# Optimization experiments

Hardware: AMD Instinct MI355X
Metric: run time of the kernel (lower is better)

## Reference

```python
import jax, jax.numpy as jnp
import numpy as np

H = 128; D = 16; L = 4
NP_ = 50000; NL_ = 10000; EPP = 500000; ELP = 100000; EPL = 100000


def _rbf(d):
    # GaussianSmearing(start=0, stop=8, num_gaussians=16)
    off = jnp.linspace(0.0, 8.0, D)
    coeff = -0.5 / ((8.0 / (D - 1)) ** 2)
    x = d[:, None] - off[None, :]
    return jnp.exp(coeff * x * x)


def _layer_norm(x, w, b, eps=1e-5):
    mu = jnp.mean(x, axis=-1, keepdims=True)
    var = jnp.var(x, axis=-1, keepdims=True)
    return (x - mu) * jax.lax.rsqrt(var + eps) * w + b


def _block(x_src, x_dst, src, dst, ea, Wf_, bf_, Ws_, bs_, bnw, bnb, lnw, lnb):
    # CGConv message: z = [x_i(dst), x_j(src), edge_attr]
    z = jnp.concatenate([x_dst[dst], x_src[src], ea], axis=-1)  # [E, 2H+D]
    m = jax.nn.sigmoid(z @ Wf_ + bf_) * jax.nn.softplus(z @ Ws_ + bs_)
    agg = jax.ops.segment_sum(m, dst, num_segments=x_dst.shape[0])
    # BatchNorm1d in eval mode with running_mean=0, running_var=1
    agg = agg * (bnw / jnp.sqrt(1.0 + 1e-5)) + bnb
    out = agg + x_dst            # CGConv internal residual
    out = _layer_norm(out, lnw, lnb)
    out = jax.nn.relu(out)
    return out + x_dst           # ResidualCGConvBlock residual (dropout=identity in eval)


def setup_inputs() -> dict:
    key = jax.random.key(0)
    ks = jax.random.split(key, 16)
    s = lambda n: 1.0 / np.sqrt(n)
    inp = {
        'x_protein': jax.random.normal(ks[0], (NP_, 6), jnp.float32),
        'x_ligand': jax.random.normal(ks[1], (NL_, 6), jnp.float32),
        'ei_pp': jnp.stack([jax.random.randint(ks[2], (EPP,), 0, NP_),
                            jax.random.randint(ks[3], (EPP,), 0, NP_)]).astype(jnp.int32),
        'ea_pp': jax.random.uniform(ks[4], (EPP,), jnp.float32, 0.0, 8.0),
        'ei_lp': jnp.stack([jax.random.randint(ks[5], (ELP,), 0, NL_),
                            jax.random.randint(ks[6], (ELP,), 0, NP_)]).astype(jnp.int32),
        'ea_lp': jax.random.uniform(ks[7], (ELP,), jnp.float32, 0.0, 8.0),
        'ei_pl': jnp.stack([jax.random.randint(ks[8], (EPL,), 0, NP_),
                            jax.random.randint(ks[9], (EPL,), 0, NL_)]).astype(jnp.int32),
        'ea_pl': jax.random.uniform(ks[10], (EPL,), jnp.float32, 0.0, 8.0),
        'Wp': jax.random.normal(ks[11], (6, H), jnp.float32) * s(6),
        'bp': jnp.zeros((H,), jnp.float32),
        'Wl': jax.random.normal(ks[12], (6, H), jnp.float32) * s(6),
        'bl': jnp.zeros((H,), jnp.float32),
        'Wf': jax.random.normal(ks[13], (L, 3, 2 * H + D, H), jnp.float32) * s(2 * H + D),
        'bf': jnp.zeros((L, 3, H), jnp.float32),
        'Ws': jax.random.normal(ks[14], (L, 3, 2 * H + D, H), jnp.float32) * s(2 * H + D),
        'bs': jnp.zeros((L, 3, H), jnp.float32),
        'bn_w': jnp.ones((L, 3, H), jnp.float32),
        'bn_b': jnp.zeros((L, 3, H), jnp.float32),
        'ln_w': jnp.ones((L, 3, H), jnp.float32),
        'ln_b': jnp.zeros((L, 3, H), jnp.float32),
        'lno_w': jnp.ones((H,), jnp.float32),
        'lno_b': jnp.zeros((H,), jnp.float32),
        'fc_w': jax.random.normal(ks[15], (H, 21), jnp.float32) * s(H),
        'fc_b': jnp.zeros((21,), jnp.float32),
    }
    return inp


def reference(x_protein, x_ligand, ei_pp, ea_pp, ei_lp, ea_lp, ei_pl, ea_pl,
              Wp, bp, Wl, bl, Wf, bf, Ws, bs, bn_w, bn_b, ln_w, ln_b,
              lno_w, lno_b, fc_w, fc_b):
    xp = x_protein @ Wp + bp
    xl = x_ligand @ Wl + bl
    rpp = _rbf(ea_pp); rlp = _rbf(ea_lp); rpl = _rbf(ea_pl)
    for l in range(L):
        # HeteroConv aggr='sum': protein receives from pp and lp; ligand from pl
        p_pp = _block(xp, xp, ei_pp[0], ei_pp[1], rpp, Wf[l, 0], bf[l, 0], Ws[l, 0], bs[l, 0],
                      bn_w[l, 0], bn_b[l, 0], ln_w[l, 0], ln_b[l, 0])
        p_lp = _block(xl, xp, ei_lp[0], ei_lp[1], rlp, Wf[l, 1], bf[l, 1], Ws[l, 1], bs[l, 1],
                      bn_w[l, 1], bn_b[l, 1], ln_w[l, 1], ln_b[l, 1])
        l_pl = _block(xp, xl, ei_pl[0], ei_pl[1], rpl, Wf[l, 2], bf[l, 2], Ws[l, 2], bs[l, 2],
                      bn_w[l, 2], bn_b[l, 2], ln_w[l, 2], ln_b[l, 2])
        xp, xl = p_pp + p_lp, l_pl
    out = _layer_norm(xp, lno_w, lno_b)
    return out @ fc_w + fc_b
```

## Files before the change

### kernel.cpp

```cpp
#include <hip/hip_runtime.h>
#include <hip/hip_bf16.h>
#include <math.h>

#define H 128
#define LOG2E 1.44269504f

typedef __bf16 bf16x8 __attribute__((ext_vector_type(8)));
typedef float f32x4 __attribute__((ext_vector_type(4)));
typedef float f32x2 __attribute__((ext_vector_type(2)));
typedef __hip_bfloat16 bf16;
typedef unsigned int uint32;

static __device__ __forceinline__ float bf2f(bf16 v){ return __bfloat162float(v); }
static __device__ __forceinline__ bf16 f2bf(float v){ return __float2bfloat16(v); }
static __device__ __forceinline__ float u2f_lo(uint32 v){ return __uint_as_float(v << 16); }
static __device__ __forceinline__ float u2f_hi(uint32 v){ return __uint_as_float(v & 0xffff0000u); }

union bfpack { struct { bf16 lo, hi; } h; uint32 u; };
static __device__ __forceinline__ uint32 pack_bf2(float a, float b){
  bfpack p; p.h.lo = f2bf(a); p.h.hi = f2bf(b); return p.u;
}

static __device__ __forceinline__ int unperm64(int r){
  int base = r & ~63; int g = r & 63; int t = g >> 4; int j = g & 15;
  return base + 4*j + t;
}

#define NBIN 256
#define PREP_WP_N (4*1024*128)
#define PREP_WL_N (4*512*128)
#define RBF_N     (12*(NBIN+1)*128)

__global__ void prep_all(const float* __restrict__ Wf, const float* __restrict__ Ws,
                         const float* __restrict__ bfv, const float* __restrict__ bsv,
                         bf16* __restrict__ Wt_p, float* __restrict__ Bias_p,
                         bf16* __restrict__ Wt_l, float* __restrict__ Bias_l,
                         bf16* __restrict__ T2,
                         const float* __restrict__ Xp, const float* __restrict__ Wp,
                         const float* __restrict__ bp, float* __restrict__ Xpo,
                         bf16* __restrict__ Xpb, int NP,
                         const float* __restrict__ Xl, const float* __restrict__ Wl,
                         const float* __restrict__ bl, float* __restrict__ Xlo,
                         bf16* __restrict__ Xlb, int NL){
  int t = blockIdx.x*blockDim.x + threadIdx.x;
  if (t < PREP_WP_N){
    int k = t & 127; int idx = t >> 7;
    int rs = idx & 1023; int l = idx >> 10;
    int r = unperm64(rs);
    int rel, c, row0; const float* W; float bias = 0.f;
    if (r < 256)      { rel=0; c=r>>1;        row0=128; W = (r&1)?Ws:Wf; }
    else if (r < 512) { rel=2; c=(r-256)>>1;  row0=128; W = (r&1)?Ws:Wf; }
    else if (r < 640) { rel=0; c=r-512; row0=0; W=Wf; bias = bfv[(l*3+rel)*H+c]; }
    else if (r < 768) { rel=0; c=r-640; row0=0; W=Ws; bias = bsv[(l*3+rel)*H+c]; }
    else if (r < 896) { rel=1; c=r-768; row0=0; W=Wf; bias = bfv[(l*3+rel)*H+c]; }
    else              { rel=1; c=r-896; row0=0; W=Ws; bias = bsv[(l*3+rel)*H+c]; }
    Wt_p[t] = f2bf(LOG2E * W[((size_t)(l*3+rel)*272 + row0 + k)*H + c]);
    if (k == 0) Bias_p[l*1024 + r] = LOG2E * bias;
    return;
  }
  t -= PREP_WP_N;
  if (t < PREP_WL_N){
    int k = t & 127; int idx = t >> 7;
    int rs = idx & 511; int l = idx >> 9;
    int r = unperm64(rs);
    int rel, c, row0; const float* W; float bias = 0.f;
    if (r < 256)      { rel=1; c=r>>1;   row0=128; W = (r&1)?Ws:Wf; }
    else if (r < 384) { rel=2; c=r-256; row0=0; W=Wf; bias = bfv[(l*3+rel)*H+c]; }
    else              { rel=2; c=r-384; row0=0; W=Ws; bias = bsv[(l*3+rel)*H+c]; }
    Wt_l[t] = f2bf(LOG2E * W[((size_t)(l*3+rel)*272 + row0 + k)*H + c]);
    if (k == 0) Bias_l[l*512 + r] = LOG2E * bias;
    return;
  }
  t -= PREP_WL_N;
  if (t < RBF_N){
    int c = t & 127;
    int b = (t >> 7) % (NBIN+1);
    int pr = t / ((NBIN+1)*128);
    float d0 = (float)b * (8.0f/(float)NBIN);
    const float* wf = Wf + ((size_t)pr*272 + 256)*H + c;
    const float* ws = Ws + ((size_t)pr*272 + 256)*H + c;
    float f0=0.f, s0=0.f;
    #pragma unroll
    for (int k=0;k<16;k++){
      float o = 0.533333333f*(float)k;
      float tt = d0 - o;
      float r0 = __expf(-1.7578125f*tt*tt);
      f0 += r0*wf[(size_t)k*H]; s0 += r0*ws[(size_t)k*H];
    }
    bf16* o = T2 + ((size_t)(pr*(NBIN+1) + b))*256 + 2*c;
    o[0]=f2bf(LOG2E * f0); o[1]=f2bf(LOG2E * s0);
    return;
  }
  t -= RBF_N;
  {
    int idx = t;
    const float* Xin; const float* W; const float* b; float* Xout; bf16* Xbf;
    if (idx < NP*H){ Xin=Xp; W=Wp; b=bp; Xout=Xpo; Xbf=Xpb; }
    else { idx -= NP*H; if (idx >= NL*H) return; Xin=Xl; W=Wl; b=bl; Xout=Xlo; Xbf=Xlb; }
    int n = idx >> 7, c = idx & 127;
    float acc = b[c];
    #pragma unroll
    for (int k=0;k<6;k++) acc += Xin[n*6+k] * W[k*H+c];
    Xout[idx] = acc;
    Xbf[idx] = f2bf(acc);
  }
}

__global__ void hist3_k(const int* __restrict__ dpp, int Epp,
                        const int* __restrict__ dlp, int Elp,
                        const int* __restrict__ dpl, int Epl,
                        int* __restrict__ cpp, int* __restrict__ clp, int* __restrict__ cpl){
  int e = blockIdx.x*blockDim.x + threadIdx.x;
  if (e < Epp) atomicAdd(&cpp[dpp[e]], 1);
  else if (e < Epp+Elp) atomicAdd(&clp[dlp[e-Epp]], 1);
  else if (e < Epp+Elp+Epl) atomicAdd(&cpl[dpl[e-Epp-Elp]], 1);
}

#define SCH 1024

__global__ void __launch_bounds__(256) chunksum_k(
    const int* __restrict__ counts, int NP, int NL, int Cpp, int Cpl,
    int* __restrict__ chsum){
  __shared__ int wred[4];
  int b = blockIdx.x;
  const int* cnt; int n; int ch;
  if (b < Cpp){ cnt = counts; n = NP; ch = b; }
  else if (b < 2*Cpp){ cnt = counts + NP; n = NP; ch = b - Cpp; }
  else { cnt = counts + 2*NP; n = NL; ch = b - 2*Cpp; }
  int base = ch * SCH;
  int tid = threadIdx.x;
  int s = 0;
  #pragma unroll
  for (int j=0;j<SCH/256;j++){
    int i = base + tid + j*256;
    if (i < n) s += cnt[i];
  }
  #pragma unroll
  for (int o=32;o>=1;o>>=1) s += __shfl_xor(s,o,64);
  if ((tid & 63) == 0) wred[tid>>6] = s;
  __syncthreads();
  if (tid == 0) chsum[b] = wred[0]+wred[1]+wred[2]+wred[3];
}

__global__ void __launch_bounds__(192) scanmid_k(
    int* __restrict__ chsum, int Cpp, int Cpl, int NP, int NL,
    int* __restrict__ rp_pp, int* __restrict__ rp_lp, int* __restrict__ rp_pl){
  int wid = threadIdx.x >> 6, lane = threadIdx.x & 63;
  int C, off; int* rp_end; int n;
  if (wid == 0){ C = Cpp; off = 0;      rp_end = rp_pp; n = NP; }
  else if (wid == 1){ C = Cpp; off = Cpp; rp_end = rp_lp; n = NP; }
  else { C = Cpl; off = 2*Cpp; rp_end = rp_pl; n = NL; }
  int v = (lane < C) ? chsum[off + lane] : 0;
  int x = v;
  #pragma unroll
  for (int o=1;o<64;o<<=1){
    int y = __shfl_up(x, o, 64);
    if (lane >= o) x += y;
// ... 79 lines not shown
    if (d > 63) d = 63;
    atomicAdd(&lh[64 + 63 - d], 1);
  }
  __syncthreads();
  if (t < 128 && lh[t]) atomicAdd(&hist[t], lh[t]);
}

__global__ void __launch_bounds__(128) degbin_scan(
    const int* __restrict__ hist, int* __restrict__ cursor){
  int t = threadIdx.x, lane = t & 63;
  int v = hist[t];
  int x = v;
  #pragma unroll
  for (int o=1;o<64;o<<=1){
    int y = __shfl_up(x, o, 64);
    if (lane >= o) x += y;
  }
  cursor[t] = x - v;
}

__global__ void __launch_bounds__(256) degbin_scatter(
    const int* __restrict__ rp_pp, const int* __restrict__ rp_lp,
    const int* __restrict__ rp_pl, int NP, int NL,
    int* __restrict__ cursor, int* __restrict__ perm){
  __shared__ int lh[128], lbase[128], lrank[128];
  int t = threadIdx.x;
  if (t < 128){ lh[t] = 0; lrank[t] = 0; }
  __syncthreads();
  int i = blockIdx.x*256 + t;
  int bin = -1, n = 0;
  if (i < NP){
    n = i;
    int d = (rp_pp[i+1]-rp_pp[i]) + (rp_lp[i+1]-rp_lp[i]);
    if (d > 63) d = 63;
    bin = 63 - d;
  } else if (i < NP+NL){
    n = i - NP;
    int d = rp_pl[n+1]-rp_pl[n];
    if (d > 63) d = 63;
    bin = 64 + 63 - d;
  }
  if (bin >= 0) atomicAdd(&lh[bin], 1);
  __syncthreads();
  if (t < 128 && lh[t]) lbase[t] = atomicAdd(&cursor[t], lh[t]);
  __syncthreads();
  if (bin >= 0){
    int r = atomicAdd(&lrank[bin], 1);
    perm[(bin < 64 ? 0 : NP) + lbase[bin] + r] = n;
  }
}

#define GR 8
__global__ void __launch_bounds__(256) gemm_tables(
    const bf16* __restrict__ Xp, const bf16* __restrict__ Wtp,
    const float* __restrict__ Biasp, bf16* __restrict__ Outp,
    int strips_p, int tasks_p,
    const bf16* __restrict__ Xl, const bf16* __restrict__ Wtl,
    const float* __restrict__ Biasl, bf16* __restrict__ Outl,
    int strips_l, int tasks_total){
  int wt = blockIdx.x*4 + (threadIdx.x >> 6);
  if (wt >= tasks_total) return;
  const bf16 *X, *Wt; const float* Bias; bf16* Out; int N, strips, g, chunk;
  if (wt < tasks_p){
    X=Xp; Wt=Wtp; Bias=Biasp; Out=Outp; N=1024; strips=strips_p;
    g = wt & 15; chunk = wt >> 4;
  } else {
    int w = wt - tasks_p;
    X=Xl; Wt=Wtl; Bias=Biasl; Out=Outl; N=512; strips=strips_l;
    g = w & 7; chunk = w >> 3;
  }
  int n0 = g << 6;
  int lane = threadIdx.x & 63;
  int lr = lane & 15, lq = lane >> 4;
  const bf16x8* B0 = (const bf16x8*)(const void*)(Wt + (size_t)(n0      + lr)*H);
  const bf16x8* B1 = (const bf16x8*)(const void*)(Wt + (size_t)(n0 + 16 + lr)*H);
  const bf16x8* B2 = (const bf16x8*)(const void*)(Wt + (size_t)(n0 + 32 + lr)*H);
  const bf16x8* B3 = (const bf16x8*)(const void*)(Wt + (size_t)(n0 + 48 + lr)*H);
  bf16x8 b0_0=B0[lq], b0_1=B0[4+lq], b0_2=B0[8+lq], b0_3=B0[12+lq];
  bf16x8 b1_0=B1[lq], b1_1=B1[4+lq], b1_2=B1[8+lq], b1_3=B1[12+lq];
  bf16x8 b2_0=B2[lq], b2_1=B2[4+lq], b2_2=B2[8+lq], b2_3=B2[12+lq];
  bf16x8 b3_0=B3[lq], b3_1=B3[4+lq], b3_2=B3[8+lq], b3_3=B3[12+lq];
  float4 bias = ((const float4*)(const void*)(Bias + n0))[lr];
  #pragma unroll 2
  for (int r=0;r<GR;r++){
    int strip = chunk*GR + r;
    if (strip >= strips) break;
    int m0 = strip << 4;
    const bf16x8* A = (const bf16x8*)(const void*)(X + (size_t)(m0+lr)*H);
    bf16x8 a0 = A[lq], a1 = A[4+lq], a2 = A[8+lq], a3 = A[12+lq];
    f32x4 acc0 = {0.f,0.f,0.f,0.f}, acc1 = acc0, acc2 = acc0, acc3 = acc0;
    acc0 = __builtin_amdgcn_mfma_f32_16x16x32_bf16(a0, b0_0, acc0, 0, 0, 0);
    acc1 = __builtin_amdgcn_mfma_f32_16x16x32_bf16(a0, b1_0, acc1, 0, 0, 0);
    acc2 = __builtin_amdgcn_mfma_f32_16x16x32_bf16(a0, b2_0, acc2, 0, 0, 0);
    acc3 = __builtin_amdgcn_mfma_f32_16x16x32_bf16(a0, b3_0, acc3, 0, 0, 0);
    acc0 = __builtin_amdgcn_mfma_f32_16x16x32_bf16(a1, b0_1, acc0, 0, 0, 0);
    acc1 = __builtin_amdgcn_mfma_f32_16x16x32_bf16(a1, b1_1, acc1, 0, 0, 0);
    acc2 = __builtin_amdgcn_mfma_f32_16x16x32_bf16(a1, b2_1, acc2, 0, 0, 0);
    acc3 = __builtin_amdgcn_mfma_f32_16x16x32_bf16(a1, b3_1, acc3, 0, 0, 0);
    acc0 = __builtin_amdgcn_mfma_f32_16x16x32_bf16(a2, b0_2, acc0, 0, 0, 0);
    acc1 = __builtin_amdgcn_mfma_f32_16x16x32_bf16(a2, b1_2, acc1, 0, 0, 0);
    acc2 = __builtin_amdgcn_mfma_f32_16x16x32_bf16(a2, b2_2, acc2, 0, 0, 0);
    acc3 = __builtin_amdgcn_mfma_f32_16x16x32_bf16(a2, b3_2, acc3, 0, 0, 0);
    acc0 = __builtin_amdgcn_mfma_f32_16x16x32_bf16(a3, b0_3, acc0, 0, 0, 0);
    acc1 = __builtin_amdgcn_mfma_f32_16x16x32_bf16(a3, b1_3, acc1, 0, 0, 0);
    acc2 = __builtin_amdgcn_mfma_f32_16x16x32_bf16(a3, b2_3, acc2, 0, 0, 0);
    acc3 = __builtin_amdgcn_mfma_f32_16x16x32_bf16(a3, b3_3, acc3, 0, 0, 0);
    #pragma unroll
    for (int rr=0;rr<4;rr++){
      int row = m0 + lq*4 + rr;
      uint2 pk;
      pk.x = pack_bf2(acc0[rr] + bias.x, acc1[rr] + bias.y);
      pk.y = pack_bf2(acc2[rr] + bias.z, acc3[rr] + bias.w);
      *(uint2*)(void*)(Out + (size_t)row*N + n0 + 4*lr) = pk;
    }
  }
}

static __device__ __forceinline__ float act_msg(float F, float S){
  float sig = __builtin_amdgcn_rcpf(1.f + __builtin_amdgcn_exp2f(-F));
  float e   = __builtin_amdgcn_exp2f(fminf(S, 86.f));
  float sp  = 0.69314718f * __builtin_amdgcn_logf(1.f + e);
  return sig * sp;
}

#define BN_RSQ 0.9999950000374997f

static __device__ __forceinline__ void edge_nb(uint2 g, uint2 t,
                                               f32x2 fd2, f32x2 sd2, f32x2& acc){
  f32x2 f2, s2;
  f2.x = u2f_lo(g.x) + u2f_lo(t.x);
  f2.y = u2f_lo(g.y) + u2f_lo(t.y);
  s2.x = u2f_hi(g.x) + u2f_hi(t.x);
  s2.y = u2f_hi(g.y) + u2f_hi(t.y);
  f2 += fd2; s2 += sd2;
  acc.x += act_msg(f2.x, s2.x);
  acc.y += act_msg(f2.y, s2.y);
}

static __device__ __forceinline__ void ln_stats_w(float v0, float v1, float& mu, float& var){
  float s = v0 + v1, q = v0*v0 + v1*v1;
  #pragma unroll
  for (int o=32;o>=1;o>>=1){ s += __shfl_xor(s,o,64); q += __shfl_xor(q,o,64); }
  mu = s * (1.f/128.f);
  var = q * (1.f/128.f) - mu*mu;
}

static __device__ __forceinline__ void aggregate(
    const int2* __restrict__ ev_arr, int e0, int e1,
    const uint2* __restrict__ G, int gstride, int goff,
    const uint2* __restrict__ Tb, int lane,
    f32x2 fd2, f32x2 sd2, f32x2& acc)
{
  for (int base = e0; base < e1; base += 64){
    int idx = base + lane;
    int2 ev = ev_arr[(idx < e1) ? idx : (e1-1)];
    float dd = __int_as_float(ev.y);
    int bnv = (int)__fmaf_rn(dd, (float)NBIN/8.0f, 0.5f);
    bnv = (bnv > NBIN) ? NBIN : bnv;
    int cnt = e1 - base; cnt = (cnt > 64) ? 64 : cnt;
    uint2 gA, tA, gB, tB, gC, tC;
    #define LDJ(gX, tX, j) { \
      int s_ = __builtin_amdgcn_readlane(ev.x, (j)); \
      int b_ = __builtin_amdgcn_readlane(bnv, (j)); \
      gX = G[(size_t)s_*gstride + goff + lane]; \
      tX = Tb[(size_t)b_*64 + lane]; }
    LDJ(gA, tA, 0);
    if (cnt > 1) LDJ(gB, tB, 1);
    if (cnt > 2) LDJ(gC, tC, 2);
    int j = 0;
    for (; j+5 < cnt; j += 3){
      edge_nb(gA, tA, fd2, sd2, acc); LDJ(gA, tA, j+3);
      edge_nb(gB, tB, fd2, sd2, acc); LDJ(gB, tB, j+4);
      edge_nb(gC, tC, fd2, sd2, acc); LDJ(gC, tC, j+5);
    }
    int rem = cnt - j;
    edge_nb(gA, tA, fd2, sd2, acc);
    if (rem > 3) LDJ(gA, tA, j+3);
    if (rem > 1) edge_nb(gB, tB, fd2, sd2, acc);
    if (rem > 4) LDJ(gB, tB, j+4);
    if (rem > 2) edge_nb(gC, tC, fd2, sd2, acc);
    if (rem > 3) edge_nb(gA, tA, fd2, sd2, acc);
    if (rem > 4) edge_nb(gB, tB, fd2, sd2, acc);
    #undef LDJ
  }
}

__global__ void __launch_bounds__(256) node_update(
    const bf16* __restrict__ PT, const bf16* __restrict__ LT,
    const float* __restrict__ xp, const float* __restrict__ xl,
    const int* __restrict__ pp_rp, const int2* __restrict__ pp_e2,
    const int* __restrict__ lp_rp, const int2* __restrict__ lp_e2,
    const int* __restrict__ pl_rp, const int2* __restrict__ pl_e2,
    const bf16* __restrict__ T2,
    const float* __restrict__ bn_w, const float* __restrict__ bn_b,
    const float* __restrict__ ln_w, const float* __restrict__ ln_b,
    const int* __restrict__ perm,
    float* __restrict__ xp_out, bf16* __restrict__ xp_bf,
    float* __restrict__ xl_out, bf16* __restrict__ xl_bf,
    int layer, int NP, int NL, int PB)
{
  int wave = threadIdx.x >> 6;
  int lane = threadIdx.x & 63;
  const uint2* PTg = (const uint2*)(const void*)PT;
  if ((int)blockIdx.x < PB){
    int idx = blockIdx.x*4 + wave;
    if (idx >= NP) return;
    int node = perm[idx];
    float2 x = ((const float2*)(const void*)(xp + (size_t)node*H))[lane];
    const uint32* PTu = (const uint32*)(const void*)PT;
    const uint2*  LTg = (const uint2*)(const void*)LT;
    float o1_0, o1_1, o2_0, o2_1;
    {
      int pr = layer*3 + 0;
      uint32 fdp = PTu[(size_t)node*512 + 256 + lane];
      uint32 sdp = PTu[(size_t)node*512 + 320 + lane];
      const uint2* Tb = (const uint2*)(const void*)(T2 + (size_t)pr*(NBIN+1)*256);
      f32x2 fd2 = {u2f_lo(fdp), u2f_hi(fdp)};
      f32x2 sd2 = {u2f_lo(sdp), u2f_hi(sdp)};
      f32x2 acc = {0.f, 0.f};
      aggregate(pp_e2, pp_rp[node], pp_rp[node+1], PTg, 256, 0, Tb, lane, fd2, sd2, acc);
      float2 bw = ((const float2*)(const void*)(bn_w + pr*H))[lane];
      float2 bb = ((const float2*)(const void*)(bn_b + pr*H))[lane];
      float2 lw = ((const float2*)(const void*)(ln_w + pr*H))[lane];
      float2 lb = ((const float2*)(const void*)(ln_b + pr*H))[lane];
      float v0 = acc.x * (bw.x * BN_RSQ) + bb.x + x.x;
      float v1 = acc.y * (bw.y * BN_RSQ) + bb.y + x.y;
      float mu, var; ln_stats_w(v0, v1, mu, var);
      float rs = rsqrtf(var + 1e-5f);
      o1_0 = fmaxf((v0-mu)*rs*lw.x + lb.x, 0.f) + x.x;
      o1_1 = fmaxf((v1-mu)*rs*lw.y + lb.y, 0.f) + x.y;
    }
    {
      int pr = layer*3 + 1;
      uint32 fdp = PTu[(size_t)node*512 + 384 + lane];
      uint32 sdp = PTu[(size_t)node*512 + 448 + lane];
      const uint2* Tb = (const uint2*)(const void*)(T2 + (size_t)pr*(NBIN+1)*256);
      f32x2 fd2 = {u2f_lo(fdp), u2f_hi(fdp)};
      f32x2 sd2 = {u2f_lo(sdp), u2f_hi(sdp)};
      f32x2 acc = {0.f, 0.f};
      aggregate(lp_e2, lp_rp[node], lp_rp[node+1], LTg, 128, 0, Tb, lane, fd2, sd2, acc);
      float2 bw = ((const float2*)(const void*)(bn_w + pr*H))[lane];
      float2 bb = ((const float2*)(const void*)(bn_b + pr*H))[lane];
      float2 lw = ((const float2*)(const void*)(ln_w + pr*H))[lane];
      float2 lb = ((const float2*)(const void*)(ln_b + pr*H))[lane];
      float v0 = acc.x * (bw.x * BN_RSQ) + bb.x + x.x;
      float v1 = acc.y * (bw.y * BN_RSQ) + bb.y + x.y;
      float mu, var; ln_stats_w(v0, v1, mu, var);
      float rs = rsqrtf(var + 1e-5f);
      o2_0 = fmaxf((v0-mu)*rs*lw.x + lb.x, 0.f) + x.x;
      o2_1 = fmaxf((v1-mu)*rs*lw.y + lb.y, 0.f) + x.y;
    }
    float out0 = o1_0 + o2_0, out1 = o1_1 + o2_1;
    ((float2*)(void*)(xp_out + (size_t)node*H))[lane] = make_float2(out0, out1);
    ((uint32*)(void*)(xp_bf + (size_t)node*H))[lane] = pack_bf2(out0, out1);
  } else {
    int idx = (blockIdx.x - PB)*4 + wave;
    if (idx >= NL) return;
    int node = perm[NP + idx];
    float2 x = ((const float2*)(const void*)(xl + (size_t)node*H))[lane];
    const uint32* LTu = (const uint32*)(const void*)LT;
    int pr = layer*3 + 2;
    uint32 fdp = LTu[(size_t)node*256 + 128 + lane];
    uint32 sdp = LTu[(size_t)node*256 + 192 + lane];
    const uint2* Tb = (const uint2*)(const void*)(T2 + (size_t)pr*(NBIN+1)*256);
    f32x2 fd2 = {u2f_lo(fdp), u2f_hi(fdp)};
    f32x2 sd2 = {u2f_lo(sdp), u2f_hi(sdp)};
    f32x2 acc = {0.f, 0.f};
    aggregate(pl_e2, pl_rp[node], pl_rp[node+1], PTg, 256, 64, Tb, lane, fd2, sd2, acc);
    float2 bw = ((const float2*)(const void*)(bn_w + pr*H))[lane];
    float2 bb = ((const float2*)(const void*)(bn_b + pr*H))[lane];
    float2 lw = ((const float2*)(const void*)(ln_w + pr*H))[lane];
    float2 lb = ((const float2*)(const void*)(ln_b + pr*H))[lane];
    float v0 = acc.x * (bw.x * BN_RSQ) + bb.x + x.x;
    float v1 = acc.y * (bw.y * BN_RSQ) + bb.y + x.y;
    float mu, var; ln_stats_w(v0, v1, mu, var);
    float rs = rsqrtf(var + 1e-5f);
    float out0 = fmaxf((v0-mu)*rs*lw.x + lb.x, 0.f) + x.x;
    float out1 = fmaxf((v1-mu)*rs*lw.y + lb.y, 0.f) + x.y;
    ((float2*)(void*)(xl_out + (size_t)node*H))[lane] = make_float2(out0, out1);
    ((uint32*)(void*)(xl_bf + (size_t)node*H))[lane] = pack_bf2(out0, out1);
  }
}

__global__ void __launch_bounds__(128) final_k(const float* __restrict__ xp,
    const float* __restrict__ lnw, const float* __restrict__ lnb,
    const float* __restrict__ fcw, const float* __restrict__ fcb,
    float* __restrict__ out, int N){
  __shared__ float sm[4];
  __shared__ float lnv[128];
  int node = blockIdx.x, c = threadIdx.x;
  float v = xp[(size_t)node*H + c];
  float s = v, q = v*v;
  #pragma unroll
  for (int o=32;o>=1;o>>=1){ s += __shfl_xor(s,o,64); q += __shfl_xor(q,o,64); }
  __syncthreads();
  if ((c & 63) == 0){ sm[(c>>6)*2] = s; sm[(c>>6)*2+1] = q; }
  __syncthreads();
  float S = sm[0] + sm[2], Q = sm[1] + sm[3];
  float mu = S * (1.f/128.f);
  float var = Q * (1.f/128.f) - mu*mu;
  float ln = (v-mu)*rsqrtf(var+1e-5f)*lnw[c] + lnb[c];
  lnv[c] = ln;
  __syncthreads();
  if (c < 21){
    float a = fcb[c];
    #pragma unroll 4
    for (int i=0;i<128;i++) a += lnv[i]*fcw[i*21+c];
    out[(size_t)node*21 + c] = a;
  }
}

extern "C" void kernel_launch(void* const* d_in, const int* in_sizes, int n_in,
                              void* d_out, int out_size, void* d_ws, size_t ws_size,
                              hipStream_t stream){
  const float* x_protein = (const float*)d_in[0];
  const float* x_ligand  = (const float*)d_in[1];
  const int*   ei_pp = (const int*)d_in[2];
  const float* ea_pp = (const float*)d_in[3];
  const int*   ei_lp = (const int*)d_in[4];
  const float* ea_lp = (const float*)d_in[5];
  const int*   ei_pl = (const int*)d_in[6];
  const float* ea_pl = (const float*)d_in[7];
  const float* Wp  = (const float*)d_in[8];
  const float* bp  = (const float*)d_in[9];
  const float* Wl  = (const float*)d_in[10];
  const float* bl  = (const float*)d_in[11];
  const float* Wf  = (const float*)d_in[12];
  const float* bfv = (const float*)d_in[13];
  const float* Wsv = (const float*)d_in[14];
  const float* bsv = (const float*)d_in[15];
  const float* bn_w = (const float*)d_in[16];
  const float* bn_b = (const float*)d_in[17];
  const float* ln_w = (const float*)d_in[18];
  const float* ln_b = (const float*)d_in[19];
  const float* lno_w = (const float*)d_in[20];
  const float* lno_b = (const float*)d_in[21];
  const float* fc_w = (const float*)d_in[22];
  const float* fc_b = (const float*)d_in[23];

  int NP  = in_sizes[0]/6, NL = in_sizes[1]/6;
  int EPP = in_sizes[3], ELP = in_sizes[5], EPL = in_sizes[7];

  char* ws = (char*)d_ws;
  size_t off = 0;
  auto alloc = [&](size_t bytes)->void*{
    void* p = ws + off; off = (off + bytes + 255) & ~(size_t)255; return p;
  };

  float* xpA = (float*)alloc((size_t)NP*H*4);
  float* xpB = (float*)alloc((size_t)NP*H*4);
  float* xlA = (float*)alloc((size_t)NL*H*4);
  float* xlB = (float*)alloc((size_t)NL*H*4);
  bf16* xp_bf = (bf16*)alloc((size_t)NP*H*2);
  bf16* xl_bf = (bf16*)alloc((size_t)NL*H*2);
  bf16* PT    = (bf16*)alloc((size_t)NP*1024*2);
  bf16* LT    = (bf16*)alloc((size_t)NL*512*2);
  bf16* Wt_p  = (bf16*)alloc((size_t)4*1024*H*2);
  bf16* Wt_l  = (bf16*)alloc((size_t)4*512*H*2);
  float* Bias_p = (float*)alloc((size_t)4*1024*4);
  float* Bias_l = (float*)alloc((size_t)4*512*4);
  bf16* T2    = (bf16*)alloc((size_t)12*(NBIN+1)*256*2);
  int* counts = (int*)alloc((size_t)(2*NP+NL)*4);
  int* rp_pp  = (int*)alloc((size_t)(NP+1)*4);
  int* cur_pp = (int*)alloc((size_t)NP*4);
  int* rp_lp  = (int*)alloc((size_t)(NP+1)*4);
  int* cur_lp = (int*)alloc((size_t)NP*4);
  int* rp_pl  = (int*)alloc((size_t)(NL+1)*4);
  int* cur_pl = (int*)alloc((size_t)NL*4);
  int2* e2_pp = (int2*)alloc((size_t)EPP*8);
  int2* e2_lp = (int2*)alloc((size_t)ELP*8);
  int2* e2_pl = (int2*)alloc((size_t)EPL*8);
  int Cpp = (NP + SCH - 1) / SCH;
  int Cpl = (NL + SCH - 1) / SCH;
  int* chsum = (int*)alloc((size_t)(2*Cpp + Cpl)*4);
  int* dhist  = (int*)alloc(128*4);
  int* dcur   = (int*)alloc(128*4);
  int* perm   = (int*)alloc((size_t)(NP+NL)*4);
  (void)ws_size; (void)n_in; (void)out_size;

  size_t prep_total = (size_t)PREP_WP_N + PREP_WL_N + RBF_N + (size_t)(NP+NL)*H;
  prep_all<<<(prep_total+255)/256, 256, 0, stream>>>(Wf, Wsv, bfv, bsv,
      Wt_p, Bias_p, Wt_l, Bias_l, T2,
      x_protein, Wp, bp, xpA, xp_bf, NP,
      x_ligand,  Wl, bl, xlA, xl_bf, NL);
  hipMemsetAsync(counts, 0, (size_t)(2*NP+NL)*4, stream);
  hipMemsetAsync(dhist, 0, 128*4, stream);
  int* cnt_pp = counts; int* cnt_lp = counts + NP; int* cnt_pl = counts + 2*NP;
  int Etot = EPP + ELP + EPL;
  hist3_k<<<(Etot+255)/256, 256, 0, stream>>>(ei_pp+EPP, EPP, ei_lp+ELP, ELP, ei_pl+EPL, EPL,
                                              cnt_pp, cnt_lp, cnt_pl);
  chunksum_k<<<2*Cpp + Cpl, 256, 0, stream>>>(counts, NP, NL, Cpp, Cpl, chsum);
  scanmid_k<<<1, 192, 0, stream>>>(chsum, Cpp, Cpl, NP, NL, rp_pp, rp_lp, rp_pl);
  scanfin_k<<<2*Cpp + Cpl, 1024, 0, stream>>>(counts, NP, NL, Cpp, Cpl, chsum,
                                              rp_pp, cur_pp, rp_lp, cur_lp, rp_pl, cur_pl);
  fill3_k<<<(Etot+255)/256, 256, 0, stream>>>(ei_pp, ea_pp, EPP, ei_lp, ea_lp, ELP,
                                              ei_pl, ea_pl, EPL,
                                              cur_pp, e2_pp, cur_lp, e2_lp, cur_pl, e2_pl);
  int nbks = (NP + NL + 255) / 256;
  degbin_hist<<<nbks, 256, 0, stream>>>(rp_pp, rp_lp, rp_pl, NP, NL, dhist);
  degbin_scan<<<1, 128, 0, stream>>>(dhist, dcur);
  degbin_scatter<<<nbks, 256, 0, stream>>>(rp_pp, rp_lp, rp_pl, NP, NL, dcur, perm);

  float* xp_cur = xpA; float* xp_nxt = xpB;
  float* xl_cur = xlA; float* xl_nxt = xlB;
  int strips_p = NP >> 4, strips_l = NL >> 4;
  int tasks_p = 16 * ((strips_p + GR - 1) / GR);
  int tasks_l = 8  * ((strips_l + GR - 1) / GR);
  int tasks_total = tasks_p + tasks_l;
  int PB = (NP + 3) / 4, LB = (NL + 3) / 4;
  for (int l=0; l<4; l++){
    gemm_tables<<<(tasks_total+3)/4, 256, 0, stream>>>(
        xp_bf, Wt_p + (size_t)l*1024*H, Bias_p + l*1024, PT, strips_p, tasks_p,
        xl_bf, Wt_l + (size_t)l*512*H,  Bias_l + l*512,  LT, strips_l, tasks_total);
    node_update<<<PB + LB, 256, 0, stream>>>(PT, LT, xp_cur, xl_cur,
        rp_pp, e2_pp, rp_lp, e2_lp, rp_pl, e2_pl, T2,
        bn_w, bn_b, ln_w, ln_b, perm, xp_nxt, xp_bf, xl_nxt, xl_bf, l, NP, NL, PB);
    float* t;
    t = xp_cur; xp_cur = xp_nxt; xp_nxt = t;
    t = xl_cur; xl_cur = xl_nxt; xl_nxt = t;
  }

  final_k<<<NP, 128, 0, stream>>>(xp_cur, lno_w, lno_b, fc_w, fc_b, (float*)d_out, NP);
}
```

Baseline: 822.5 us.

## Switch node tables and features from bf16/fp32 to fp16 with packed half adds

Converts the per-layer gather tables, weights, RBF tables and node features from bf16 (plus an fp32 copy) to fp16. The GEMM now uses the f16 MFMA, and the per-edge message sum is done with packed half2 adds instead of unpacking to fp32. The separate fp32 feature buffers are dropped and the residual is read from fp16, which cuts memory traffic. The table column interleave is also reordered so that f and s halves pack into adjacent uint32 words. The cost is fp16 range and precision risk in the residual stream and in the pre-activation sums.

```diff
diff --git a/kernel.cpp b/kernel.cpp
--- a/kernel.cpp
+++ b/kernel.cpp
@@ -5,20 +5,17 @@
 #define H 128
 #define LOG2E 1.44269504f
 
-typedef __bf16 bf16x8 __attribute__((ext_vector_type(8)));
+typedef _Float16 f16;
+typedef _Float16 f16x2 __attribute__((ext_vector_type(2)));
+typedef _Float16 f16x8 __attribute__((ext_vector_type(8)));
 typedef float f32x4 __attribute__((ext_vector_type(4)));
 typedef float f32x2 __attribute__((ext_vector_type(2)));
-typedef __hip_bfloat16 bf16;
 typedef unsigned int uint32;
 
-static __device__ __forceinline__ float bf2f(bf16 v){ return __bfloat162float(v); }
-static __device__ __forceinline__ bf16 f2bf(float v){ return __float2bfloat16(v); }
-static __device__ __forceinline__ float u2f_lo(uint32 v){ return __uint_as_float(v << 16); }
-static __device__ __forceinline__ float u2f_hi(uint32 v){ return __uint_as_float(v & 0xffff0000u); }
-
-union bfpack { struct { bf16 lo, hi; } h; uint32 u; };
-static __device__ __forceinline__ uint32 pack_bf2(float a, float b){
-  bfpack p; p.h.lo = f2bf(a); p.h.hi = f2bf(b); return p.u;
+union u2h { uint32 u; f16x2 h; };
+static __device__ __forceinline__ f16x2 as_h2(uint32 v){ u2h x; x.u = v; return x.h; }
+static __device__ __forceinline__ uint32 pack_h2(float a, float b){
+  u2h p; p.h = (f16x2){(f16)a, (f16)b}; return p.u;
 }
 
 static __device__ __forceinline__ int unperm64(int r){
@@ -33,28 +30,31 @@
 
 __global__ void prep_all(const float* __restrict__ Wf, const float* __restrict__ Ws,
                          const float* __restrict__ bfv, const float* __restrict__ bsv,
-                         bf16* __restrict__ Wt_p, float* __restrict__ Bias_p,
-                         bf16* __restrict__ Wt_l, float* __restrict__ Bias_l,
-                         bf16* __restrict__ T2,
+                         f16* __restrict__ Wt_p, float* __restrict__ Bias_p,
+                         f16* __restrict__ Wt_l, float* __restrict__ Bias_l,
+                         f16* __restrict__ T2,
                          const float* __restrict__ Xp, const float* __restrict__ Wp,
-                         const float* __restrict__ bp, float* __restrict__ Xpo,
-                         bf16* __restrict__ Xpb, int NP,
+                         const float* __restrict__ bp, f16* __restrict__ Xph, int NP,
                          const float* __restrict__ Xl, const float* __restrict__ Wl,
-                         const float* __restrict__ bl, float* __restrict__ Xlo,
-                         bf16* __restrict__ Xlb, int NL){
+                         const float* __restrict__ bl, f16* __restrict__ Xlh, int NL){
   int t = blockIdx.x*blockDim.x + threadIdx.x;
   if (t < PREP_WP_N){
     int k = t & 127; int idx = t >> 7;
     int rs = idx & 1023; int l = idx >> 10;
     int r = unperm64(rs);
     int rel, c, row0; const float* W; float bias = 0.f;
-    if (r < 256)      { rel=0; c=r>>1;        row0=128; W = (r&1)?Ws:Wf; }
-    else if (r < 512) { rel=2; c=(r-256)>>1;  row0=128; W = (r&1)?Ws:Wf; }
+    if (r < 512){
+      rel = (r < 256) ? 0 : 2;
+      int rr = r & 255; int j = rr & 3;
+      W = (j >= 2) ? Ws : Wf;
+      c = ((rr >> 2) << 1) | (j & 1);
+      row0 = 128;
+    }
     else if (r < 640) { rel=0; c=r-512; row0=0; W=Wf; bias = bfv[(l*3+rel)*H+c]; }
     else if (r < 768) { rel=0; c=r-640; row0=0; W=Ws; bias = bsv[(l*3+rel)*H+c]; }
     else if (r < 896) { rel=1; c=r-768; row0=0; W=Wf; bias = bfv[(l*3+rel)*H+c]; }
     else              { rel=1; c=r-896; row0=0; W=Ws; bias = bsv[(l*3+rel)*H+c]; }
-    Wt_p[t] = f2bf(LOG2E * W[((size_t)(l*3+rel)*272 + row0 + k)*H + c]);
+    Wt_p[t] = (f16)(LOG2E * W[((size_t)(l*3+rel)*272 + row0 + k)*H + c]);
     if (k == 0) Bias_p[l*1024 + r] = LOG2E * bias;
     return;
   }
@@ -64,10 +64,15 @@
     int rs = idx & 511; int l = idx >> 9;
     int r = unperm64(rs);
     int rel, c, row0; const float* W; float bias = 0.f;
-    if (r < 256)      { rel=1; c=r>>1;   row0=128; W = (r&1)?Ws:Wf; }
+    if (r < 256){
+      rel = 1; int j = r & 3;
+      W = (j >= 2) ? Ws : Wf;
+      c = ((r >> 2) << 1) | (j & 1);
+      row0 = 128;
+    }
     else if (r < 384) { rel=2; c=r-256; row0=0; W=Wf; bias = bfv[(l*3+rel)*H+c]; }
     else              { rel=2; c=r-384; row0=0; W=Ws; bias = bsv[(l*3+rel)*H+c]; }
-    Wt_l[t] = f2bf(LOG2E * W[((size_t)(l*3+rel)*272 + row0 + k)*H + c]);
+    Wt_l[t] = (f16)(LOG2E * W[((size_t)(l*3+rel)*272 + row0 + k)*H + c]);
     if (k == 0) Bias_l[l*512 + r] = LOG2E * bias;
     return;
   }
@@ -87,22 +92,23 @@
       float r0 = __expf(-1.7578125f*tt*tt);
       f0 += r0*wf[(size_t)k*H]; s0 += r0*ws[(size_t)k*H];
     }
-    bf16* o = T2 + ((size_t)(pr*(NBIN+1) + b))*256 + 2*c;
-    o[0]=f2bf(LOG2E * f0); o[1]=f2bf(LOG2E * s0);
+    f16* o = T2 + ((size_t)(pr*(NBIN+1) + b))*256;
+    int m = c >> 1, sub = c & 1;
+    o[4*m + sub]     = (f16)(LOG2E * f0);
+    o[4*m + 2 + sub] = (f16)(LOG2E * s0);
     return;
   }
   t -= RBF_N;
   {
     int idx = t;
-    const float* Xin; const float* W; const float* b; float* Xout; bf16* Xbf;
-    if (idx < NP*H){ Xin=Xp; W=Wp; b=bp; Xout=Xpo; Xbf=Xpb; }
-    else { idx -= NP*H; if (idx >= NL*H) return; Xin=Xl; W=Wl; b=bl; Xout=Xlo; Xbf=Xlb; }
+    const float* Xin; const float* W; const float* b; f16* Xh;
+    if (idx < NP*H){ Xin=Xp; W=Wp; b=bp; Xh=Xph; }
+    else { idx -= NP*H; if (idx >= NL*H) return; Xin=Xl; W=Wl; b=bl; Xh=Xlh; }
     int n = idx >> 7, c = idx & 127;
     float acc = b[c];
     #pragma unroll
     for (int k=0;k<6;k++) acc += Xin[n*6+k] * W[k*H+c];
-    Xout[idx] = acc;
-    Xbf[idx] = f2bf(acc);
+    Xh[idx] = (f16)acc;
   }
 }
 
@@ -288,15 +294,15 @@
 
 #define GR 8
 __global__ void __launch_bounds__(256) gemm_tables(
-    const bf16* __restrict__ Xp, const bf16* __restrict__ Wtp,
-    const float* __restrict__ Biasp, bf16* __restrict__ Outp,
+    const f16* __restrict__ Xp, const f16* __restrict__ Wtp,
+    const float* __restrict__ Biasp, f16* __restrict__ Outp,
     int strips_p, int tasks_p,
-    const bf16* __restrict__ Xl, const bf16* __restrict__ Wtl,
-    const float* __restrict__ Biasl, bf16* __restrict__ Outl,
+    const f16* __restrict__ Xl, const f16* __restrict__ Wtl,
+    const float* __restrict__ Biasl, f16* __restrict__ Outl,
     int strips_l, int tasks_total){
   int wt = blockIdx.x*4 + (threadIdx.x >> 6);
   if (wt >= tasks_total) return;
-  const bf16 *X, *Wt; const float* Bias; bf16* Out; int N, strips, g, chunk;
+  const f16 *X, *Wt; const float* Bias; f16* Out; int N, strips, g, chunk;
   if (wt < tasks_p){
     X=Xp; Wt=Wtp; Bias=Biasp; Out=Outp; N=1024; strips=strips_p;
     g = wt & 15; chunk = wt >> 4;
@@ -308,45 +314,45 @@
   int n0 = g << 6;
   int lane = threadIdx.x & 63;
   int lr = lane & 15, lq = lane >> 4;
-  const bf16x8* B0 = (const bf16x8*)(const void*)(Wt + (size_t)(n0      + lr)*H);
-  const bf16x8* B1 = (const bf16x8*)(const void*)(Wt + (size_t)(n0 + 16 + lr)*H);
-  const bf16x8* B2 = (const bf16x8*)(const void*)(Wt + (size_t)(n0 + 32 + lr)*H);
-  const bf16x8* B3 = (const bf16x8*)(const void*)(Wt + (size_t)(n0 + 48 + lr)*H);
-  bf16x8 b0_0=B0[lq], b0_1=B0[4+lq], b0_2=B0[8+lq], b0_3=B0[12+lq];
-  bf16x8 b1_0=B1[lq], b1_1=B1[4+lq], b1_2=B1[8+lq], b1_3=B1[12+lq];
-  bf16x8 b2_0=B2[lq], b2_1=B2[4+lq], b2_2=B2[8+lq], b2_3=B2[12+lq];
-  bf16x8 b3_0=B3[lq], b3_1=B3[4+lq], b3_2=B3[8+lq], b3_3=B3[12+lq];
+  const f16x8* B0 = (const f16x8*)(const void*)(Wt + (size_t)(n0      + lr)*H);
+  const f16x8* B1 = (const f16x8*)(const void*)(Wt + (size_t)(n0 + 16 + lr)*H);
+  const f16x8* B2 = (const f16x8*)(const void*)(Wt + (size_t)(n0 + 32 + lr)*H);
+  const f16x8* B3 = (const f16x8*)(const void*)(Wt + (size_t)(n0 + 48 + lr)*H);
+  f16x8 b0_0=B0[lq], b0_1=B0[4+lq], b0_2=B0[8+lq], b0_3=B0[12+lq];
+  f16x8 b1_0=B1[lq], b1_1=B1[4+lq], b1_2=B1[8+lq], b1_3=B1[12+lq];
+  f16x8 b2_0=B2[lq], b2_1=B2[4+lq], b2_2=B2[8+lq], b2_3=B2[12+lq];
+  f16x8 b3_0=B3[lq], b3_1=B3[4+lq], b3_2=B3[8+lq], b3_3=B3[12+lq];
   float4 bias = ((const float4*)(const void*)(Bias + n0))[lr];
   #pragma unroll 2
   for (int r=0;r<GR;r++){
     int strip = chunk*GR + r;
     if (strip >= strips) break;
     int m0 = strip << 4;
-    const bf16x8* A = (const bf16x8*)(const void*)(X + (size_t)(m0+lr)*H);
-    bf16x8 a0 = A[lq], a1 = A[4+lq], a2 = A[8+lq], a3 = A[12+lq];
+    const f16x8* A = (const f16x8*)(const void*)(X + (size_t)(m0+lr)*H);
+    f16x8 a0 = A[lq], a1 = A[4+lq], a2 = A[8+lq], a3 = A[12+lq];
     f32x4 acc0 = {0.f,0.f,0.f,0.f}, acc1 = acc0, acc2 = acc0, acc3 = acc0;
-    acc0 = __builtin_amdgcn_mfma_f32_16x16x32_bf16(a0, b0_0, acc0, 0, 0, 0);
-    acc1 = __builtin_amdgcn_mfma_f32_16x16x32_bf16(a0, b1_0, acc1, 0, 0, 0);
-    acc2 = __builtin_amdgcn_mfma_f32_16x16x32_bf16(a0, b2_0, acc2, 0, 0, 0);
-    acc3 = __builtin_amdgcn_mfma_f32_16x16x32_bf16(a0, b3_0, acc3, 0, 0, 0);
-    acc0 = __builtin_amdgcn_mfma_f32_16x16x32_bf16(a1, b0_1, acc0, 0, 0, 0);
-    acc1 = __builtin_amdgcn_mfma_f32_16x16x32_bf16(a1, b1_1, acc1, 0, 0, 0);
-    acc2 = __builtin_amdgcn_mfma_f32_16x16x32_bf16(a1, b2_1, acc2, 0, 0, 0);
-    acc3 = __builtin_amdgcn_mfma_f32_16x16x32_bf16(a1, b3_1, acc3, 0, 0, 0);
-    acc0 = __builtin_amdgcn_mfma_f32_16x16x32_bf16(a2, b0_2, acc0, 0, 0, 0);
-    acc1 = __builtin_amdgcn_mfma_f32_16x16x32_bf16(a2, b1_2, acc1, 0, 0, 0);
-    acc2 = __builtin_amdgcn_mfma_f32_16x16x32_bf16(a2, b2_2, acc2, 0, 0, 0);
-    acc3 = __builtin_amdgcn_mfma_f32_16x16x32_bf16(a2, b3_2, acc3, 0, 0, 0);
-    acc0 = __builtin_amdgcn_mfma_f32_16x16x32_bf16(a3, b0_3, acc0, 0, 0, 0);
-    acc1 = __builtin_amdgcn_mfma_f32_16x16x32_bf16(a3, b1_3, acc1, 0, 0, 0);
-    acc2 = __builtin_amdgcn_mfma_f32_16x16x32_bf16(a3, b2_3, acc2, 0, 0, 0);
-    acc3 = __builtin_amdgcn_mfma_f32_16x16x32_bf16(a3, b3_3, acc3, 0, 0, 0);
+    acc0 = __builtin_amdgcn_mfma_f32_16x16x32_f16(a0, b0_0, acc0, 0, 0, 0);
+    acc1 = __builtin_amdgcn_mfma_f32_16x16x32_f16(a0, b1_0, acc1, 0, 0, 0);
+    acc2 = __builtin_amdgcn_mfma_f32_16x16x32_f16(a0, b2_0, acc2, 0, 0, 0);
+    acc3 = __builtin_amdgcn_mfma_f32_16x16x32_f16(a0, b3_0, acc3, 0, 0, 0);
+    acc0 = __builtin_amdgcn_mfma_f32_16x16x32_f16(a1, b0_1, acc0, 0, 0, 0);
+    acc1 = __builtin_amdgcn_mfma_f32_16x16x32_f16(a1, b1_1, acc1, 0, 0, 0);
+    acc2 = __builtin_amdgcn_mfma_f32_16x16x32_f16(a1, b2_1, acc2, 0, 0, 0);
+    acc3 = __builtin_amdgcn_mfma_f32_16x16x32_f16(a1, b3_1, acc3, 0, 0, 0);
+    acc0 = __builtin_amdgcn_mfma_f32_16x16x32_f16(a2, b0_2, acc0, 0, 0, 0);
+    acc1 = __builtin_amdgcn_mfma_f32_16x16x32_f16(a2, b1_2, acc1, 0, 0, 0);
+    acc2 = __builtin_amdgcn_mfma_f32_16x16x32_f16(a2, b2_2, acc2, 0, 0, 0);
+    acc3 = __builtin_amdgcn_mfma_f32_16x16x32_f16(a2, b3_2, acc3, 0, 0, 0);
+    acc0 = __builtin_amdgcn_mfma_f32_16x16x32_f16(a3, b0_3, acc0, 0, 0, 0);
+    acc1 = __builtin_amdgcn_mfma_f32_16x16x32_f16(a3, b1_3, acc1, 0, 0, 0);
+    acc2 = __builtin_amdgcn_mfma_f32_16x16x32_f16(a3, b2_3, acc2, 0, 0, 0);
+    acc3 = __builtin_amdgcn_mfma_f32_16x16x32_f16(a3, b3_3, acc3, 0, 0, 0);
     #pragma unroll
     for (int rr=0;rr<4;rr++){
       int row = m0 + lq*4 + rr;
       uint2 pk;
-      pk.x = pack_bf2(acc0[rr] + bias.x, acc1[rr] + bias.y);
-      pk.y = pack_bf2(acc2[rr] + bias.z, acc3[rr] + bias.w);
+      pk.x = pack_h2(acc0[rr] + bias.x, acc1[rr] + bias.y);
+      pk.y = pack_h2(acc2[rr] + bias.z, acc3[rr] + bias.w);
       *(uint2*)(void*)(Out + (size_t)row*N + n0 + 4*lr) = pk;
     }
   }
@@ -362,15 +368,11 @@
 #define BN_RSQ 0.9999950000374997f
 
 static __device__ __forceinline__ void edge_nb(uint2 g, uint2 t,
-                                               f32x2 fd2, f32x2 sd2, f32x2& acc){
-  f32x2 f2, s2;
-  f2.x = u2f_lo(g.x) + u2f_lo(t.x);
-  f2.y = u2f_lo(g.y) + u2f_lo(t.y);
-  s2.x = u2f_hi(g.x) + u2f_hi(t.x);
-  s2.y = u2f_hi(g.y) + u2f_hi(t.y);
-  f2 += fd2; s2 += sd2;
-  acc.x += act_msg(f2.x, s2.x);
-  acc.y += act_msg(f2.y, s2.y);
+                                               f16x2 fd2, f16x2 sd2, f32x2& acc){
+  f16x2 F = (as_h2(g.x) + as_h2(t.x)) + fd2;
+  f16x2 S = (as_h2(g.y) + as_h2(t.y)) + sd2;
+  acc.x += act_msg((float)F.x, (float)S.x);
+  acc.y += act_msg((float)F.y, (float)S.y);
 }
 
 static __device__ __forceinline__ void ln_stats_w(float v0, float v1, float& mu, float& var){
@@ -385,7 +387,7 @@
     const int2* __restrict__ ev_arr, int e0, int e1,
     const uint2* __restrict__ G, int gstride, int goff,
     const uint2* __restrict__ Tb, int lane,
-    f32x2 fd2, f32x2 sd2, f32x2& acc)
+    f16x2 fd2, f16x2 sd2, f32x2& acc)
 {
   for (int base = e0; base < e1; base += 64){
     int idx = base + lane;
@@ -422,17 +424,16 @@
 }
 
 __global__ void __launch_bounds__(256) node_update(
-    const bf16* __restrict__ PT, const bf16* __restrict__ LT,
-    const float* __restrict__ xp, const float* __restrict__ xl,
+    const f16* __restrict__ PT, const f16* __restrict__ LT,
+    const f16* __restrict__ xp, const f16* __restrict__ xl,
     const int* __restrict__ pp_rp, const int2* __restrict__ pp_e2,
     const int* __restrict__ lp_rp, const int2* __restrict__ lp_e2,
     const int* __restrict__ pl_rp, const int2* __restrict__ pl_e2,
-    const bf16* __restrict__ T2,
+    const f16* __restrict__ T2,
     const float* __restrict__ bn_w, const float* __restrict__ bn_b,
     const float* __restrict__ ln_w, const float* __restrict__ ln_b,
     const int* __restrict__ perm,
-    float* __restrict__ xp_out, bf16* __restrict__ xp_bf,
-    float* __restrict__ xl_out, bf16* __restrict__ xl_bf,
+    f16* __restrict__ xp_o, f16* __restrict__ xl_o,
     int layer, int NP, int NL, int PB)
 {
   int wave = threadIdx.x >> 6;
@@ -442,90 +443,84 @@
     int idx = blockIdx.x*4 + wave;
     if (idx >= NP) return;
     int node = perm[idx];
-    float2 x = ((const float2*)(const void*)(xp + (size_t)node*H))[lane];
+    f16x2 xh = as_h2(((const uint32*)(const void*)xp)[(size_t)node*64 + lane]);
+    float xx = (float)xh.x, xy = (float)xh.y;
     const uint32* PTu = (const uint32*)(const void*)PT;
     const uint2*  LTg = (const uint2*)(const void*)LT;
     float o1_0, o1_1, o2_0, o2_1;
     {
       int pr = layer*3 + 0;
-      uint32 fdp = PTu[(size_t)node*512 + 256 + lane];
-      uint32 sdp = PTu[(size_t)node*512 + 320 + lane];
+      f16x2 fd2 = as_h2(PTu[(size_t)node*512 + 256 + lane]);
+      f16x2 sd2 = as_h2(PTu[(size_t)node*512 + 320 + lane]);
       const uint2* Tb = (const uint2*)(const void*)(T2 + (size_t)pr*(NBIN+1)*256);
-      f32x2 fd2 = {u2f_lo(fdp), u2f_hi(fdp)};
-      f32x2 sd2 = {u2f_lo(sdp), u2f_hi(sdp)};
       f32x2 acc = {0.f, 0.f};
       aggregate(pp_e2, pp_rp[node], pp_rp[node+1], PTg, 256, 0, Tb, lane, fd2, sd2, acc);
       float2 bw = ((const float2*)(const void*)(bn_w + pr*H))[lane];
       float2 bb = ((const float2*)(const void*)(bn_b + pr*H))[lane];
       float2 lw = ((const float2*)(const void*)(ln_w + pr*H))[lane];
       float2 lb = ((const float2*)(const void*)(ln_b + pr*H))[lane];
-      float v0 = acc.x * (bw.x * BN_RSQ) + bb.x + x.x;
-      float v1 = acc.y * (bw.y * BN_RSQ) + bb.y + x.y;
+      float v0 = acc.x * (bw.x * BN_RSQ) + bb.x + xx;
+      float v1 = acc.y * (bw.y * BN_RSQ) + bb.y + xy;
       float mu, var; ln_stats_w(v0, v1, mu, var);
       float rs = rsqrtf(var + 1e-5f);
-      o1_0 = fmaxf((v0-mu)*rs*lw.x + lb.x, 0.f) + x.x;
-      o1_1 = fmaxf((v1-mu)*rs*lw.y + lb.y, 0.f) + x.y;
+      o1_0 = fmaxf((v0-mu)*rs*lw.x + lb.x, 0.f) + xx;
+      o1_1 = fmaxf((v1-mu)*rs*lw.y + lb.y, 0.f) + xy;
     }
     {
       int pr = layer*3 + 1;
-      uint32 fdp = PTu[(size_t)node*512 + 384 + lane];
-      uint32 sdp = PTu[(size_t)node*512 + 448 + lane];
+      f16x2 fd2 = as_h2(PTu[(size_t)node*512 + 384 + lane]);
+      f16x2 sd2 = as_h2(PTu[(size_t)node*512 + 448 + lane]);
       const uint2* Tb = (const uint2*)(const void*)(T2 + (size_t)pr*(NBIN+1)*256);
-      f32x2 fd2 = {u2f_lo(fdp), u2f_hi(fdp)};
-      f32x2 sd2 = {u2f_lo(sdp), u2f_hi(sdp)};
       f32x2 acc = {0.f, 0.f};
       aggregate(lp_e2, lp_rp[node], lp_rp[node+1], LTg, 128, 0, Tb, lane, fd2, sd2, acc);
       float2 bw = ((const float2*)(const void*)(bn_w + pr*H))[lane];
       float2 bb = ((const float2*)(const void*)(bn_b + pr*H))[lane];
       float2 lw = ((const float2*)(const void*)(ln_w + pr*H))[lane];
       float2 lb = ((const float2*)(const void*)(ln_b + pr*H))[lane];
-      float v0 = acc.x * (bw.x * BN_RSQ) + bb.x + x.x;
-      float v1 = acc.y * (bw.y * BN_RSQ) + bb.y + x.y;
+      float v0 = acc.x * (bw.x * BN_RSQ) + bb.x + xx;
+      float v1 = acc.y * (bw.y * BN_RSQ) + bb.y + xy;
       float mu, var; ln_stats_w(v0, v1, mu, var);
       float rs = rsqrtf(var + 1e-5f);
-      o2_0 = fmaxf((v0-mu)*rs*lw.x + lb.x, 0.f) + x.x;
-      o2_1 = fmaxf((v1-mu)*rs*lw.y + lb.y, 0.f) + x.y;
+      o2_0 = fmaxf((v0-mu)*rs*lw.x + lb.x, 0.f) + xx;
+      o2_1 = fmaxf((v1-mu)*rs*lw.y + lb.y, 0.f) + xy;
     }
     float out0 = o1_0 + o2_0, out1 = o1_1 + o2_1;
-    ((float2*)(void*)(xp_out + (size_t)node*H))[lane] = make_float2(out0, out1);
-    ((uint32*)(void*)(xp_bf + (size_t)node*H))[lane] = pack_bf2(out0, out1);
+    ((uint32*)(void*)xp_o)[(size_t)node*64 + lane] = pack_h2(out0, out1);
   } else {
     int idx = (blockIdx.x - PB)*4 + wave;
     if (idx >= NL) return;
     int node = perm[NP + idx];
-    float2 x = ((const float2*)(const void*)(xl + (size_t)node*H))[lane];
+    f16x2 xh = as_h2(((const uint32*)(const void*)xl)[(size_t)node*64 + lane]);
+    float xx = (float)xh.x, xy = (float)xh.y;
     const uint32* LTu = (const uint32*)(const void*)LT;
     int pr = layer*3 + 2;
-    uint32 fdp = LTu[(size_t)node*256 + 128 + lane];
-    uint32 sdp = LTu[(size_t)node*256 + 192 + lane];
+    f16x2 fd2 = as_h2(LTu[(size_t)node*256 + 128 + lane]);
+    f16x2 sd2 = as_h2(LTu[(size_t)node*256 + 192 + lane]);
     const uint2* Tb = (const uint2*)(const void*)(T2 + (size_t)pr*(NBIN+1)*256);
-    f32x2 fd2 = {u2f_lo(fdp), u2f_hi(fdp)};
-    f32x2 sd2 = {u2f_lo(sdp), u2f_hi(sdp)};
     f32x2 acc = {0.f, 0.f};
     aggregate(pl_e2, pl_rp[node], pl_rp[node+1], PTg, 256, 64, Tb, lane, fd2, sd2, acc);
     float2 bw = ((const float2*)(const void*)(bn_w + pr*H))[lane];
     float2 bb = ((const float2*)(const void*)(bn_b + pr*H))[lane];
     float2 lw = ((const float2*)(const void*)(ln_w + pr*H))[lane];
     float2 lb = ((const float2*)(const void*)(ln_b + pr*H))[lane];
-    float v0 = acc.x * (bw.x * BN_RSQ) + bb.x + x.x;
-    float v1 = acc.y * (bw.y * BN_RSQ) + bb.y + x.y;
+    float v0 = acc.x * (bw.x * BN_RSQ) + bb.x + xx;
+    float v1 = acc.y * (bw.y * BN_RSQ) + bb.y + xy;
     float mu, var; ln_stats_w(v0, v1, mu, var);
     float rs = rsqrtf(var + 1e-5f);
-    float out0 = fmaxf((v0-mu)*rs*lw.x + lb.x, 0.f) + x.x;
-    float out1 = fmaxf((v1-mu)*rs*lw.y + lb.y, 0.f) + x.y;
-    ((float2*)(void*)(xl_out + (size_t)node*H))[lane] = make_float2(out0, out1);
-    ((uint32*)(void*)(xl_bf + (size_t)node*H))[lane] = pack_bf2(out0, out1);
-  }
-}
-
-__global__ void __launch_bounds__(128) final_k(const float* __restrict__ xp,
+    float out0 = fmaxf((v0-mu)*rs*lw.x + lb.x, 0.f) + xx;
+    float out1 = fmaxf((v1-mu)*rs*lw.y + lb.y, 0.f) + xy;
+    ((uint32*)(void*)xl_o)[(size_t)node*64 + lane] = pack_h2(out0, out1);
+  }
+}
+
+__global__ void __launch_bounds__(128) final_k(const f16* __restrict__ xp,
     const float* __restrict__ lnw, const float* __restrict__ lnb,
     const float* __restrict__ fcw, const float* __restrict__ fcb,
     float* __restrict__ out, int N){
   __shared__ float sm[4];
   __shared__ float lnv[128];
   int node = blockIdx.x, c = threadIdx.x;
-  float v = xp[(size_t)node*H + c];
+  float v = (float)xp[(size_t)node*H + c];
   float s = v, q = v*v;
   #pragma unroll
   for (int o=32;o>=1;o>>=1){ s += __shfl_xor(s,o,64); q += __shfl_xor(q,o,64); }
@@ -583,19 +578,17 @@
     void* p = ws + off; off = (off + bytes + 255) & ~(size_t)255; return p;
   };
 
-  float* xpA = (float*)alloc((size_t)NP*H*4);
-  float* xpB = (float*)alloc((size_t)NP*H*4);
-  float* xlA = (float*)alloc((size_t)NL*H*4);
-  float* xlB = (float*)alloc((size_t)NL*H*4);
-  bf16* xp_bf = (bf16*)alloc((size_t)NP*H*2);
-  bf16* xl_bf = (bf16*)alloc((size_t)NL*H*2);
-  bf16* PT    = (bf16*)alloc((size_t)NP*1024*2);
-  bf16* LT    = (bf16*)alloc((size_t)NL*512*2);
-  bf16* Wt_p  = (bf16*)alloc((size_t)4*1024*H*2);
-  bf16* Wt_l  = (bf16*)alloc((size_t)4*512*H*2);
+  f16* xpA = (f16*)alloc((size_t)NP*H*2);
+  f16* xpB = (f16*)alloc((size_t)NP*H*2);
+  f16* xlA = (f16*)alloc((size_t)NL*H*2);
+  f16* xlB = (f16*)alloc((size_t)NL*H*2);
+  f16* PT    = (f16*)alloc((size_t)NP*1024*2);
+  f16* LT    = (f16*)alloc((size_t)NL*512*2);
+  f16* Wt_p  = (f16*)alloc((size_t)4*1024*H*2);
+  f16* Wt_l  = (f16*)alloc((size_t)4*512*H*2);
   float* Bias_p = (float*)alloc((size_t)4*1024*4);
   float* Bias_l = (float*)alloc((size_t)4*512*4);
-  bf16* T2    = (bf16*)alloc((size_t)12*(NBIN+1)*256*2);
+  f16* T2    = (f16*)alloc((size_t)12*(NBIN+1)*256*2);
   int* counts = (int*)alloc((size_t)(2*NP+NL)*4);
   int* rp_pp  = (int*)alloc((size_t)(NP+1)*4);
   int* cur_pp = (int*)alloc((size_t)NP*4);
@@ -617,8 +610,8 @@
   size_t prep_total = (size_t)PREP_WP_N + PREP_WL_N + RBF_N + (size_t)(NP+NL)*H;
   prep_all<<<(prep_total+255)/256, 256, 0, stream>>>(Wf, Wsv, bfv, bsv,
       Wt_p, Bias_p, Wt_l, Bias_l, T2,
-      x_protein, Wp, bp, xpA, xp_bf, NP,
-      x_ligand,  Wl, bl, xlA, xl_bf, NL);
+      x_protein, Wp, bp, xpA, NP,
+      x_ligand,  Wl, bl, xlA, NL);
   hipMemsetAsync(counts, 0, (size_t)(2*NP+NL)*4, stream);
   hipMemsetAsync(dhist, 0, 128*4, stream);
   int* cnt_pp = counts; int* cnt_lp = counts + NP; int* cnt_pl = counts + 2*NP;
@@ -637,8 +630,8 @@
   degbin_scan<<<1, 128, 0, stream>>>(dhist, dcur);
   degbin_scatter<<<nbks, 256, 0, stream>>>(rp_pp, rp_lp, rp_pl, NP, NL, dcur, perm);
 
-  float* xp_cur = xpA; float* xp_nxt = xpB;
-  float* xl_cur = xlA; float* xl_nxt = xlB;
+  f16* xp_cur = xpA; f16* xp_nxt = xpB;
+  f16* xl_cur = xlA; f16* xl_nxt = xlB;
   int strips_p = NP >> 4, strips_l = NL >> 4;
   int tasks_p = 16 * ((strips_p + GR - 1) / GR);
   int tasks_l = 8  * ((strips_l + GR - 1) / GR);
@@ -646,12 +639,12 @@
   int PB = (NP + 3) / 4, LB = (NL + 3) / 4;
   for (int l=0; l<4; l++){
     gemm_tables<<<(tasks_total+3)/4, 256, 0, stream>>>(
-        xp_bf, Wt_p + (size_t)l*1024*H, Bias_p + l*1024, PT, strips_p, tasks_p,
-        xl_bf, Wt_l + (size_t)l*512*H,  Bias_l + l*512,  LT, strips_l, tasks_total);
+        xp_cur, Wt_p + (size_t)l*1024*H, Bias_p + l*1024, PT, strips_p, tasks_p,
+        xl_cur, Wt_l + (size_t)l*512*H,  Bias_l + l*512,  LT, strips_l, tasks_total);
     node_update<<<PB + LB, 256, 0, stream>>>(PT, LT, xp_cur, xl_cur,
         rp_pp, e2_pp, rp_lp, e2_lp, rp_pl, e2_pl, T2,
-        bn_w, bn_b, ln_w, ln_b, perm, xp_nxt, xp_bf, xl_nxt, xl_bf, l, NP, NL, PB);
-    float* t;
+        bn_w, bn_b, ln_w, ln_b, perm, xp_nxt, xl_nxt, l, NP, NL, PB);
+    f16* t;
     t = xp_cur; xp_cur = xp_nxt; xp_nxt = t;
     t = xl_cur; xl_cur = xl_nxt; xl_nxt = t;
   }
```

New measurement: 751.8 us. -8.6%, faster.
